# Optimization experiments

Measured on AMD Instinct MI355X. Metric: run time of the kernel, lower is better.

Reference implementation:

```python
import jax, jax.numpy as jnp
import numpy as np

B, S, N = 16, 128, 64            # batch, sentence length, padded KB-word slots per sentence
E, DK, H, L = 128, 128, 128, 32  # char embed, kb embed, per-direction hidden (hidden_size=2H), labels
CHAR_NUM, KB_NUM = 8000, 200000


def setup_inputs():
    key = jax.random.key(0)
    ks = jax.random.split(key, 40)
    u = lambda k, sh: jax.random.uniform(k, sh, jnp.float32, -0.08, 0.08)
    inp = {
        "char_ids": jax.random.randint(ks[0], (B, S), 0, CHAR_NUM),
        "kb_word_ids": jax.random.randint(ks[1], (B, N), 0, KB_NUM),
        "word_begin": jax.random.randint(ks[2], (B, N), 0, S),
        "word_len": jax.random.randint(ks[3], (B, N), 0, 6),
        "label": jax.random.randint(ks[4], (B, S), 0, L),
        "sequence_length": jax.random.randint(ks[5], (B,), S // 2, S + 1),
        "char_emb": u(ks[6], (CHAR_NUM, E)),
        "kb_emb": u(ks[7], (KB_NUM, DK)),
        "dense_W": u(ks[8], (2 * H, L)),
        "dense_b": jnp.zeros((L,), jnp.float32),
        "crf_T": u(ks[9], (L, L)),
    }
    i = 10
    for p in ("f", "r"):
        inp[p + "_Wcx"] = u(ks[i], (E, 4 * H))
        inp[p + "_Wch"] = u(ks[i + 1], (H, 4 * H))
        inp[p + "_bc"] = jnp.zeros((4 * H,), jnp.float32)
        inp[p + "_Wwx"] = u(ks[i + 2], (DK, 3 * H))
        inp[p + "_Wwh"] = u(ks[i + 3], (H, 3 * H))
        inp[p + "_bw"] = jnp.zeros((3 * H,), jnp.float32)
        inp[p + "_Wlx"] = u(ks[i + 4], (E, H))
        inp[p + "_Wlc"] = u(ks[i + 5], (H, H))
        inp[p + "_bl"] = jnp.zeros((H,), jnp.float32)
        i += 6
    return inp


def _lattice_dir(X, Xw, begin, end, pos_valid, word_valid,
                 Wcx, Wch, bc, Wwx, Wwh, bw, Wlx, Wlc, bl):
    # X:[S,E] chars in scan order, Xw:[N,DK] KB words, begin/end:[N] span indices
    # in scan order (end inclusive), pos_valid:[S] bool, word_valid:[N] bool.
    Xg = X @ Wcx + bc    # [S,4H] hoisted char-gate input projection
    Xl = X @ Wlx + bl    # [S,H]  hoisted link-gate input projection
    Wg = Xw @ Wwx + bw   # [N,3H] hoisted word-gate input projection

    def step(carry, t):
        h_hist, c_hist = carry                 # [S+1,H]; slot k = state after step k-1
        h_prev, c_prev = h_hist[t], c_hist[t]
        gi, gf, go, gg = jnp.split(Xg[t] + h_prev @ Wch, 4)
        i = jax.nn.sigmoid(gi); f = jax.nn.sigmoid(gf)
        o = jax.nn.sigmoid(go); g = jnp.tanh(gg)
        # word cells: built from the state just before each word's begin position
        hb, cb = h_hist[begin], c_hist[begin]  # [N,H]
        wi, wf, wg = jnp.split(Wg + hb @ Wwh, 3, axis=1)
        cw = jax.nn.sigmoid(wf) * cb + jax.nn.sigmoid(wi) * jnp.tanh(wg)  # [N,H]
        lg = jax.nn.sigmoid(Xl[t] + cw @ Wlc)  # [N,H] link gates
        wmask = ((end == t) & word_valid).astype(X.dtype)[:, None]
        ew = jnp.exp(lg) * wmask
        ec = jnp.exp(i)
        c_lat = (ec * g + (ew * cw).sum(0)) / (ec + ew.sum(0))  # gate-normalized merge
        c_std = f * c_prev + i * g             # plain LSTM step when no word ends at t
        c_t = jnp.where(wmask.sum() > 0, c_lat, c_std)
        h_t = o * jnp.tanh(c_t)
        v = pos_valid[t]
        h_hist = h_hist.at[t + 1].set(jnp.where(v, h_t, h_prev))
        c_hist = c_hist.at[t + 1].set(jnp.where(v, c_t, c_prev))
        return (h_hist, c_hist), jnp.where(v, h_t, jnp.zeros_like(h_t))

    init = (jnp.zeros((S + 1, H), X.dtype), jnp.zeros((S + 1, H), X.dtype))
    _, hs = jax.lax.scan(step, init, jnp.arange(S))
    return hs  # [S,H]


def _forward(char_ids, kb_word_ids, word_begin, word_len, label, sequence_length,
             char_emb, kb_emb, dense_W, dense_b, crf_T, fparams, rparams):
    X = char_emb[char_ids]            # [B,S,E]
    Xw = kb_emb[kb_word_ids]          # [B,N,DK]
    end = jnp.minimum(word_begin + word_len, S - 1)   # inclusive span end
    word_valid = end < sequence_length[:, None]       # whole span inside sentence
    pos = jnp.arange(S)
    pv_f = pos[None, :] < sequence_length[:, None]
    fwd = jax.vmap(lambda x, xw, b, e, pv, wv:
                   _lattice_dir(x, xw, b, e, pv, wv, *fparams))(
        X, Xw, word_begin, end, pv_f, word_valid)
    # backward direction: flip time axis; span (b,e) maps to (S-1-e, S-1-b)
    pv_r = pos[None, :] >= (S - sequence_length)[:, None]
    bwd = jax.vmap(lambda x, xw, b, e, pv, wv:
                   _lattice_dir(x, xw, b, e, pv, wv, *rparams))(
        X[:, ::-1], Xw, S - 1 - end, S - 1 - word_begin, pv_r, word_valid)[:, ::-1]
    feats = jnp.concatenate([fwd, bwd], axis=-1)      # [B,S,2H]
    logits = feats @ dense_W + dense_b                # [B,S,L]
    # CRF negative log-likelihood
    mask = pv_f.astype(logits.dtype)                  # [B,S]
    emit = jnp.take_along_axis(logits, label[..., None], axis=2)[..., 0]
    trans = crf_T[label[:, :-1], label[:, 1:]]
    gold = (emit * mask).sum(1) + (trans * mask[:, 1:]).sum(1)

    def fstep(alpha, xs):
        logit_t, m_t = xs
        new = jax.scipy.special.logsumexp(alpha[:, :, None] + crf_T[None], axis=1) + logit_t
        return jnp.where(m_t[:, None] > 0, new, alpha), None

    alpha, _ = jax.lax.scan(fstep, logits[:, 0],
                            (logits[:, 1:].transpose(1, 0, 2), mask[:, 1:].T))
    logZ = jax.scipy.special.logsumexp(alpha, axis=1)
    return jnp.mean(logZ - gold)


def reference(char_ids, kb_word_ids, word_begin, word_len, label, sequence_length,
              char_emb, kb_emb, dense_W, dense_b, crf_T,
              f_Wcx, f_Wch, f_bc, f_Wwx, f_Wwh, f_bw, f_Wlx, f_Wlc, f_bl,
              r_Wcx, r_Wch, r_bc, r_Wwx, r_Wwh, r_bw, r_Wlx, r_Wlc, r_bl):
    fparams = (f_Wcx, f_Wch, f_bc, f_Wwx, f_Wwh, f_bw, f_Wlx, f_Wlc, f_bl)
    rparams = (r_Wcx, r_Wch, r_bc, r_Wwx, r_Wwh, r_bw, r_Wlx, r_Wlc, r_bl)
    return _forward(char_ids, kb_word_ids, word_begin, word_len, label, sequence_length,
                    char_emb, kb_emb, dense_W, dense_b, crf_T, fparams, rparams)
```

## Files before the change

kernel.cpp:

```cpp
#include <hip/hip_runtime.h>


typedef _Float16 f16x2 __attribute__((ext_vector_type(2)));

__device__ __forceinline__ float sigm(float x) { return 1.f / (1.f + __expf(-x)); }
__device__ __forceinline__ float tanh_fast(float x) {
    return 1.f - 2.f / (__expf(2.f * x) + 1.f);
}
__device__ __forceinline__ void bar_lgkm() {
    asm volatile("s_waitcnt lgkmcnt(0)\n\ts_barrier" ::: "memory");
}

#if defined(__has_builtin)
#if __has_builtin(__builtin_amdgcn_fdot2)
#define FDOT2(a, b, c) __builtin_amdgcn_fdot2((a), (b), (c), false)
#endif
#endif
#ifndef FDOT2
__device__ __forceinline__ float fdot2_sw(f16x2 a, f16x2 b, float c) {
    return fmaf((float)a.x, (float)b.x, fmaf((float)a.y, (float)b.y, c));
}
#define FDOT2(a, b, c) fdot2_sw((a), (b), (c))
#endif

template <int K, int J, int RPB, int BLK>
__global__ __launch_bounds__(BLK)
void gemm_pair(const float* __restrict__ emb, const int* __restrict__ idx,
               const float* __restrict__ W0, const float* __restrict__ W1,
               const float* __restrict__ b0, const float* __restrict__ b1,
               float* __restrict__ out, int rowsTotal, int Sdim, int revmode)
{
    constexpr int NJ4 = J / 4;
    constexpr int RT  = BLK / NJ4;
    constexpr int RPT = RPB / RT;
    static_assert(BLK % NJ4 == 0 && RPB % RT == 0, "layout");
    const int y = blockIdx.y;
    const float* __restrict__ W    = y ? W1 : W0;
    const float* __restrict__ bias = y ? b1 : b0;
    float* __restrict__ outp = out + (size_t)y * rowsTotal * J;
    const int rev = (revmode && y) ? 1 : 0;

    __shared__ __align__(16) float xs[RPB * K];
    __shared__ const float* srcs[RPB];
    const int tid = threadIdx.x;
    const int r0 = blockIdx.x * RPB;
    if (tid < RPB) {
        const int row = r0 + tid;
        const float* s = nullptr;
        if (row < rowsTotal) {
            if (idx) {
                const int bb = row / Sdim, tt = row - bb * Sdim;
                const int ts = rev ? (Sdim - 1 - tt) : tt;
                s = emb + (size_t)idx[bb * Sdim + ts] * K;
            } else {
                s = emb + (size_t)row * K;
            }
        }
        srcs[tid] = s;
    }
    __syncthreads();
    constexpr int NQ = RPB * K / 4;
    for (int q = tid; q < NQ; q += BLK) {
        const int rr = q / (K / 4), qq = q - rr * (K / 4);
        const float4* s = (const float4*)srcs[rr];
        ((float4*)xs)[q] = s ? s[qq] : make_float4(0.f, 0.f, 0.f, 0.f);
    }
    __syncthreads();

    const int jq = tid % NJ4;
    const int rg = tid / NJ4;
    float4 acc[RPT];
#pragma unroll
    for (int r = 0; r < RPT; ++r) acc[r] = make_float4(0.f, 0.f, 0.f, 0.f);
    const float4* __restrict__ W4 = (const float4*)W;
#pragma unroll 4
    for (int k = 0; k < K; ++k) {
        const float4 wv = W4[(size_t)k * NJ4 + jq];
#pragma unroll
        for (int r = 0; r < RPT; ++r) {
            const float xv = xs[(rg * RPT + r) * K + k];
            acc[r].x = fmaf(xv, wv.x, acc[r].x);
            acc[r].y = fmaf(xv, wv.y, acc[r].y);
            acc[r].z = fmaf(xv, wv.z, acc[r].z);
            acc[r].w = fmaf(xv, wv.w, acc[r].w);
        }
    }
    const float4 bv = ((const float4*)bias)[jq];
#pragma unroll
    for (int r = 0; r < RPT; ++r) {
        const int row = r0 + rg * RPT + r;
        if (row < rowsTotal)
            ((float4*)outp)[(size_t)row * NJ4 + jq] =
                make_float4(acc[r].x + bv.x, acc[r].y + bv.y,
                            acc[r].z + bv.z, acc[r].w + bv.w);
    }
}

#define HH_BYTES (129 * 128 * 2)
#define CH_BYTES (129 * 128 * 4)
#define LAT_DYN_SMEM (HH_BYTES + CH_BYTES)

__global__ __launch_bounds__(512, 2)
void lattice_kernel(const float* __restrict__ Xg,
                    const float* __restrict__ Xl,
                    const float* __restrict__ Wgp,
                    const float* __restrict__ Wch_f, const float* __restrict__ Wch_r,
                    const float* __restrict__ Wwh_f, const float* __restrict__ Wwh_r,
                    const float* __restrict__ Wlc_f, const float* __restrict__ Wlc_r,
                    const int* __restrict__ word_begin, const int* __restrict__ word_len,
                    const int* __restrict__ seqlen,
                    float* __restrict__ feats)
{
    extern __shared__ __align__(16) char dyn_smem[];
    _Float16* hh = (_Float16*)dyn_smem;
    float*    ch = (float*)(dyn_smem + HH_BYTES);

    const int bdid = blockIdx.x;
    const int b = bdid >> 1, dir = bdid & 1;
    const int tid = threadIdx.x;
    const int kc = tid >> 7;
    const int jj = tid & 127;

    const float* Wch = dir ? Wch_r : Wch_f;
    const float* Wwh = dir ? Wwh_r : Wwh_f;
    const float* Wlc = dir ? Wlc_r : Wlc_f;

    f16x2 wch2[64];
    {
        const float* base = Wch + (size_t)(kc * 32) * 512 + jj;
#pragma unroll
        for (int g = 0; g < 4; ++g)
#pragma unroll
            for (int u2 = 0; u2 < 16; ++u2) {
                f16x2 v;
                v.x = (_Float16)base[(size_t)(2 * u2) * 512 + g * 128];
                v.y = (_Float16)base[(size_t)(2 * u2 + 1) * 512 + g * 128];
                wch2[g * 16 + u2] = v;
            }
    }
    f16x2 wwh2[48];
    {
        const float* base = Wwh + (size_t)(kc * 32) * 384 + jj;
#pragma unroll
        for (int g = 0; g < 3; ++g)
#pragma unroll
            for (int u2 = 0; u2 < 16; ++u2) {
                f16x2 v;
                v.x = (_Float16)base[(size_t)(2 * u2) * 384 + g * 128];
                v.y = (_Float16)base[(size_t)(2 * u2 + 1) * 384 + g * 128];
                wwh2[g * 16 + u2] = v;
            }
    }
    f16x2 wlc2[16];
    {
        const float* base = Wlc + (size_t)(kc * 32) * 128 + jj;
#pragma unroll
        for (int u2 = 0; u2 < 16; ++u2) {
            f16x2 v;
            v.x = (_Float16)base[(size_t)(2 * u2) * 128];
            v.y = (_Float16)base[(size_t)(2 * u2 + 1) * 128];
            wlc2[u2] = v;
        }
    }

    __shared__ __align__(16) float part[2048];
    __shared__ __align__(16) float wpart[2 * 1536];
    __shared__ __align__(16) float lpart[2 * 512];
    __shared__ __align__(16) _Float16 cw2s[2 * 128];
    __shared__ int ev_start[129];
    __shared__ int cnts[128];
    __shared__ int fills[128];
    __shared__ short ev_word[64];
    __shared__ short wbeg_s[64];

    const int sl = seqlen[b];

    if (tid < 128) { cnts[tid] = 0; fills[tid] = 0; }
    __syncthreads();
    int myvalid = 0, myed = 0;
    if (tid < 64) {
        const int bg = word_begin[b * 64 + tid];
        const int ln = word_len[b * 64 + tid];
        int ef = bg + ln; if (ef > 127) ef = 127;
        myvalid = (ef < sl);
        const int bd_ = dir ? (127 - ef) : bg;
        const int ed_ = dir ? (127 - bg) : ef;
        wbeg_s[tid] = (short)bd_;
        myed = ed_;
        if (myvalid) atomicAdd(&cnts[ed_], 1);
    }
    __syncthreads();
    if (tid == 0) {
        int run = 0; ev_start[0] = 0;
        for (int t = 0; t < 128; ++t) { run += cnts[t]; ev_start[t + 1] = run; }
    }
    __syncthreads();
    if (tid < 64 && myvalid) {
        const int pos = atomicAdd(&fills[myed], 1);
        ev_word[ev_start[myed] + pos] = (short)tid;
    }
    if (tid < 128) { hh[tid] = (_Float16)0.f; ch[tid] = 0.f; }
    __syncthreads();

    const float* Xg_b = Xg + ((size_t)dir * 2048 + (size_t)b * 128) * 512;
    const float* Xl_b = Xl + ((size_t)dir * 2048 + (size_t)b * 128) * 128;
    const float* Wg_b = Wgp + ((size_t)dir * 1024 + (size_t)b * 64) * 384;

    float h_reg = 0.f, c_reg = 0.f;
    float xg_cur = Xg_b[tid];

    for (int t = 0; t < 128; ++t) {
        const int e0 = ev_start[t];
        const int E  = ev_start[t + 1] - e0;
        const int ec0 = E < 2 ? E : 2;

        int bgs[2] = {0, 0};
        float wgp[2][3];
        float xl = 0.f;
#pragma unroll
        for (int s = 0; s < 2; ++s)
            if (s < ec0) {
                const int w = ev_word[e0 + s];
                bgs[s] = wbeg_s[w];
                if (tid < 128) {
                    const float* wgr = Wg_b + (size_t)w * 384;
                    wgp[s][0] = wgr[tid]; wgp[s][1] = wgr[128 + tid]; wgp[s][2] = wgr[256 + tid];
                }
            }
        if (E > 0 && tid < 128) xl = Xl_b[(size_t)t * 128 + tid];
        const float xg_nxt = (t < 127) ? Xg_b[(size_t)(t + 1) * 512 + tid] : 0.f;

        {
            const f16x2* hrow = (const f16x2*)(hh + (size_t)t * 128) + kc * 16;
            f16x2 hv[16];
#pragma unroll
            for (int u2 = 0; u2 < 16; ++u2) hv[u2] = hrow[u2];
            float p0 = 0.f, p1 = 0.f, p2 = 0.f, p3 = 0.f;
#pragma unroll
            for (int u2 = 0; u2 < 16; ++u2) {
                p0 = FDOT2(wch2[u2],      hv[u2], p0);
                p1 = FDOT2(wch2[16 + u2], hv[u2], p1);
                p2 = FDOT2(wch2[32 + u2], hv[u2], p2);
                p3 = FDOT2(wch2[48 + u2], hv[u2], p3);
            }
            if      (kc == 0) p0 += xg_cur;
            else if (kc == 1) p1 += xg_cur;
            else if (kc == 2) p2 += xg_cur;
            else              p3 += xg_cur;
            part[kc * 512 +       jj] = p0;
            part[kc * 512 + 128 + jj] = p1;
            part[kc * 512 + 256 + jj] = p2;
            part[kc * 512 + 384 + jj] = p3;
        }
#pragma unroll
        for (int s = 0; s < 2; ++s)
            if (s < ec0) {
                const f16x2* hbrow = (const f16x2*)(hh + (size_t)bgs[s] * 128) + kc * 16;
                float q0 = 0.f, q1 = 0.f, q2 = 0.f;
#pragma unroll
                for (int u2 = 0; u2 < 16; ++u2) {
                    const f16x2 hb = hbrow[u2];
                    q0 = FDOT2(wwh2[u2],      hb, q0);
                    q1 = FDOT2(wwh2[16 + u2], hb, q1);
                    q2 = FDOT2(wwh2[32 + u2], hb, q2);
                }
                wpart[s * 1536 + kc * 384 +       jj] = q0;
                wpart[s * 1536 + kc * 384 + 128 + jj] = q1;
                wpart[s * 1536 + kc * 384 + 256 + jj] = q2;
            }
        bar_lgkm();

        float gi = 0.f, gf = 0.f, go = 0.f, gg = 0.f;
        float cwreg[2] = {0.f, 0.f};
        if (tid < 128) {
            const float a0 = part[tid]       + part[512 + tid]  + part[1024 + tid] + part[1536 + tid];
            const float a1 = part[128 + tid] + part[640 + tid]  + part[1152 + tid] + part[1664 + tid];
            const float a2 = part[256 + tid] + part[768 + tid]  + part[1280 + tid] + part[1792 + tid];
            const float a3 = part[384 + tid] + part[896 + tid]  + part[1408 + tid] + part[1920 + tid];
            gi = sigm(a0); gf = sigm(a1); go = sigm(a2); gg = tanh_fast(a3);
#pragma unroll
            for (int s = 0; s < 2; ++s)
                if (s < ec0) {
                    const int sb = s * 1536;
                    const float cb = ch[(size_t)bgs[s] * 128 + tid];
                    const float wi = wgp[s][0] + wpart[sb + tid]       + wpart[sb + 384 + tid] + wpart[sb + 768 + tid]  + wpart[sb + 1152 + tid];
                    const float wf = wgp[s][1] + wpart[sb + 128 + tid] + wpart[sb + 512 + tid] + wpart[sb + 896 + tid]  + wpart[sb + 1280 + tid];
                    const float wv = wgp[s][2] + wpart[sb + 256 + tid] + wpart[sb + 640 + tid] + wpart[sb + 1024 + tid] + wpart[sb + 1408 + tid];
                    const float cwv = sigm(wf) * cb + sigm(wi) * tanh_fast(wv);
                    cwreg[s] = cwv;
                    cw2s[s * 128 + tid] = (_Float16)cwv;
                }
        }

        float accn = 0.f, accd = 0.f;
        if (E > 0) {
            bar_lgkm();
            const int nc = (E + 1) >> 1;
            for (int c = 0; c < nc; ++c) {
                const int base = c * 2;
                const int en = (E - base) < 2 ? (E - base) : 2;
#pragma unroll
                for (int s = 0; s < 2; ++s)
                    if (s < en) {
                        const f16x2* cwrow = (const f16x2*)(cw2s + s * 128) + kc * 16;
                        float r = 0.f;
#pragma unroll
                        for (int u2 = 0; u2 < 16; ++u2) r = FDOT2(wlc2[u2], cwrow[u2], r);
                        lpart[s * 512 + kc * 128 + jj] = r;
                    }
                const int nb = base + 2;
                int nn = E - nb; nn = nn < 0 ? 0 : (nn > 2 ? 2 : nn);
                int bgs2[2] = {0, 0};
                float wgp2[2][3];
#pragma unroll
                for (int s = 0; s < 2; ++s)
                    if (s < nn) {
                        const int w = ev_word[e0 + nb + s];
                        bgs2[s] = wbeg_s[w];
                        if (tid < 128) {
                            const float* wgr = Wg_b + (size_t)w * 384;
                            wgp2[s][0] = wgr[tid]; wgp2[s][1] = wgr[128 + tid]; wgp2[s][2] = wgr[256 + tid];
                        }
                    }
#pragma unroll
                for (int s = 0; s < 2; ++s)
                    if (s < nn) {
                        const f16x2* hbrow = (const f16x2*)(hh + (size_t)bgs2[s] * 128) + kc * 16;
                        float q0 = 0.f, q1 = 0.f, q2 = 0.f;
#pragma unroll
                        for (int u2 = 0; u2 < 16; ++u2) {
                            const f16x2 hb = hbrow[u2];
                            q0 = FDOT2(wwh2[u2],      hb, q0);
                            q1 = FDOT2(wwh2[16 + u2], hb, q1);
                            q2 = FDOT2(wwh2[32 + u2], hb, q2);
                        }
                        wpart[s * 1536 + kc * 384 +       jj] = q0;
                        wpart[s * 1536 + kc * 384 + 128 + jj] = q1;
                        wpart[s * 1536 + kc * 384 + 256 + jj] = q2;
                    }
                bar_lgkm();
                if (tid < 128) {
#pragma unroll
                    for (int s = 0; s < 2; ++s)
                        if (s < en) {
                            const float lg = sigm(xl + lpart[s * 512 + tid] + lpart[s * 512 + 128 + tid]
                                                     + lpart[s * 512 + 256 + tid] + lpart[s * 512 + 384 + tid]);
                            const float ew = __expf(lg);
                            accn = fmaf(ew, cwreg[s], accn);
                            accd += ew;
                        }
#pragma unroll
                    for (int s = 0; s < 2; ++s)
                        if (s < nn) {
                            const int sb = s * 1536;
                            const float cb = ch[(size_t)bgs2[s] * 128 + tid];
                            const float wi = wgp2[s][0] + wpart[sb + tid]       + wpart[sb + 384 + tid] + wpart[sb + 768 + tid]  + wpart[sb + 1152 + tid];
                            const float wf = wgp2[s][1] + wpart[sb + 128 + tid] + wpart[sb + 512 + tid] + wpart[sb + 896 + tid]  + wpart[sb + 1280 + tid];
                            const float wv = wgp2[s][2] + wpart[sb + 256 + tid] + wpart[sb + 640 + tid] + wpart[sb + 1024 + tid] + wpart[sb + 1408 + tid];
                            const float cwv = sigm(wf) * cb + sigm(wi) * tanh_fast(wv);
                            cwreg[s] = cwv;
                            cw2s[s * 128 + tid] = (_Float16)cwv;
                        }
                }
                if (c + 1 < nc) bar_lgkm();
            }
        }

        if (tid < 128) {
            float c_t;
            if (E > 0) {
                const float ec = __expf(gi);
                c_t = (ec * gg + accn) / (ec + accd);
            } else {
                c_t = gf * c_reg + gi * gg;
            }
            const float h_t = go * tanh_fast(c_t);
            const bool v = dir ? (t >= 128 - sl) : (t < sl);
            const float hn = v ? h_t : h_reg;
            const float cn = v ? c_t : c_reg;
            h_reg = hn; c_reg = cn;
            hh[(size_t)(t + 1) * 128 + tid] = (_Float16)hn;
            ch[(size_t)(t + 1) * 128 + tid] = cn;
        }
        xg_cur = xg_nxt;
        bar_lgkm();
    }

    for (int i = tid; i < 128 * 128; i += 512) {
        const int t = i >> 7, j = i & 127;
        const bool v = dir ? (t >= 128 - sl) : (t < sl);
        const float hv = v ? (float)hh[(size_t)(t + 1) * 128 + j] : 0.f;
        const int s = dir ? (127 - t) : t;
        feats[((size_t)b * 128 + s) * 256 + dir * 128 + j] = hv;
    }
}

__global__ void crf_kernel(const float* __restrict__ logits,
                           const int* __restrict__ label,
                           const int* __restrict__ seqlen,
                           const float* __restrict__ T,
                           float* __restrict__ out_part)
{
    const int half = threadIdx.x >> 5;
    const int j    = threadIdx.x & 31;
    const int b    = blockIdx.x * 2 + half;

    float Tc[32];
#pragma unroll
    for (int i = 0; i < 32; ++i) Tc[i] = T[i * 32 + j];

    const float* lg = logits + (size_t)b * 128 * 32;
    const int* lab = label + b * 128;
    const int sl = seqlen[b];

    float g = 0.f;
#pragma unroll
    for (int r = 0; r < 4; ++r) {
        const int t = j + r * 32;
        if (t < sl) {
            g += lg[t * 32 + lab[t]];
            if (t >= 1) g += T[lab[t - 1] * 32 + lab[t]];
        }
    }
#pragma unroll
    for (int m = 16; m; m >>= 1) g += __shfl_xor(g, m, 32);

    __shared__ __align__(16) float alpha_s[2][32];
    float av = lg[j];
    alpha_s[half][j] = av;
    __syncthreads();
    for (int t = 1; t < 128; ++t) {
        float a[32];
        const float4* ap = (const float4*)alpha_s[half];
#pragma unroll
        for (int q = 0; q < 8; ++q) {
            const float4 v = ap[q];
            a[4 * q] = v.x; a[4 * q + 1] = v.y; a[4 * q + 2] = v.z; a[4 * q + 3] = v.w;
        }
        float m = -1e30f;
#pragma unroll
        for (int i = 0; i < 32; ++i) m = fmaxf(m, a[i] + Tc[i]);
        float s = 0.f;
#pragma unroll
        for (int i = 0; i < 32; ++i) s += __expf(a[i] + Tc[i] - m);
        float nv = m + __logf(s) + lg[t * 32 + j];
        if (t >= sl) nv = av;
        av = nv;
        __syncthreads();
        alpha_s[half][j] = av;
        __syncthreads();
    }
    float m2 = av;
#pragma unroll
    for (int m = 16; m; m >>= 1) m2 = fmaxf(m2, __shfl_xor(m2, m, 32));
    float s2 = __expf(av - m2);
#pragma unroll
    for (int m = 16; m; m >>= 1) s2 += __shfl_xor(s2, m, 32);
    if (j == 0) out_part[b] = (m2 + __logf(s2)) - g;
}

__global__ void finalize_kernel(const float* __restrict__ partb, float* __restrict__ out)
{
    if (threadIdx.x == 0 && blockIdx.x == 0) {
        float s = 0.f;
        for (int i = 0; i < 16; i++) s += partb[i];
        out[0] = s * (1.f / 16.f);
    }
}

extern "C" void kernel_launch(void* const* d_in, const int* in_sizes, int n_in,
                              void* d_out, int out_size, void* d_ws, size_t ws_size,
                              hipStream_t stream)
{
    (void)in_sizes; (void)n_in; (void)out_size; (void)ws_size;
    const int*   char_ids    = (const int*)d_in[0];
    const int*   kb_word_ids = (const int*)d_in[1];
    const int*   word_begin  = (const int*)d_in[2];
    const int*   word_len    = (const int*)d_in[3];
    const int*   label       = (const int*)d_in[4];
    const int*   seqlen      = (const int*)d_in[5];
    const float* char_emb    = (const float*)d_in[6];
    const float* kb_emb      = (const float*)d_in[7];
    const float* dense_W     = (const float*)d_in[8];
    const float* dense_b     = (const float*)d_in[9];
    const float* crf_T       = (const float*)d_in[10];
    const float* f_Wcx = (const float*)d_in[11];
    const float* f_Wch = (const float*)d_in[12];
    const float* f_bc  = (const float*)d_in[13];
    const float* f_Wwx = (const float*)d_in[14];
    const float* f_Wwh = (const float*)d_in[15];
    const float* f_bw  = (const float*)d_in[16];
    const float* f_Wlx = (const float*)d_in[17];
    const float* f_Wlc = (const float*)d_in[18];
    const float* f_bl  = (const float*)d_in[19];
    const float* r_Wcx = (const float*)d_in[20];
    const float* r_Wch = (const float*)d_in[21];
    const float* r_bc  = (const float*)d_in[22];
    const float* r_Wwx = (const float*)d_in[23];
    const float* r_Wwh = (const float*)d_in[24];
    const float* r_bw  = (const float*)d_in[25];
    const float* r_Wlx = (const float*)d_in[26];
    const float* r_Wlc = (const float*)d_in[27];
    const float* r_bl  = (const float*)d_in[28];

    float* ws = (float*)d_ws;
    size_t o = 0;
    float* Xg     = ws + o; o += (size_t)2 * 2048 * 512;
    float* Xl     = ws + o; o += (size_t)2 * 2048 * 128;
    float* Wg     = ws + o; o += (size_t)2 * 1024 * 384;
    float* feats  = ws + o; o += (size_t)2048 * 256;
    float* logits = ws + o; o += (size_t)2048 * 32;
    float* partb  = ws + o; o += 16;

    gemm_pair<128, 512, 8, 256><<<dim3(256, 2), 256, 0, stream>>>(
        char_emb, char_ids, f_Wcx, r_Wcx, f_bc, r_bc, Xg, 2048, 128, 1);
    gemm_pair<128, 128, 8, 256><<<dim3(256, 2), 256, 0, stream>>>(
        char_emb, char_ids, f_Wlx, r_Wlx, f_bl, r_bl, Xl, 2048, 128, 1);
    gemm_pair<128, 384, 8, 192><<<dim3(128, 2), 192, 0, stream>>>(
        kb_emb, kb_word_ids, f_Wwx, r_Wwx, f_bw, r_bw, Wg, 1024, 64, 0);

    lattice_kernel<<<32, 512, LAT_DYN_SMEM, stream>>>(
        Xg, Xl, Wg, f_Wch, r_Wch, f_Wwh, r_Wwh, f_Wlc, r_Wlc,
        word_begin, word_len, seqlen, feats);

    gemm_pair<256, 32, 16, 128><<<dim3(128, 1), 128, 0, stream>>>(
        feats, nullptr, dense_W, dense_W, dense_b, dense_b, logits, 2048, 128, 0);
    crf_kernel<<<8, 64, 0, stream>>>(logits, label, seqlen, crf_T, partb);
    finalize_kernel<<<1, 64, 0, stream>>>(partb, (float*)d_out);
}
```

Measured before the change: 540.6 us.

## Move word-cell weights to LDS, ring-buffer h/c history, stream feats per step

The lattice kernel no longer keeps the word-cell recurrent weights (Wwh) in per-thread registers; they are staged once into dynamic LDS as fp16 pairs, which cuts VGPR pressure, and a waves_per_eu attribute is added. The full 129-step h/c history in LDS is replaced by an 8-slot ring window. This is only correct while every word span reaches back fewer than 8 steps, which holds because word_len is below 6. Each step now writes its hidden output straight to feats instead of running a separate copy loop at the end. The projection GEMMs also move to 32-row tiles with fewer blocks. The trade-off is extra LDS reads on the word path in exchange for fewer registers and less end-of-kernel work.

```diff
diff --git a/kernel.cpp b/kernel.cpp
--- a/kernel.cpp
+++ b/kernel.cpp
@@ -96,11 +96,9 @@
     }
 }
 
-#define HH_BYTES (129 * 128 * 2)
-#define CH_BYTES (129 * 128 * 4)
-#define LAT_DYN_SMEM (HH_BYTES + CH_BYTES)
-
-__global__ __launch_bounds__(512, 2)
+#define WWH_LDS_BYTES (64 * 384 * 4)
+
+__global__ __launch_bounds__(512, 2) __attribute__((amdgpu_waves_per_eu(2, 2)))
 void lattice_kernel(const float* __restrict__ Xg,
                     const float* __restrict__ Xl,
                     const float* __restrict__ Wgp,
@@ -112,8 +110,7 @@
                     float* __restrict__ feats)
 {
     extern __shared__ __align__(16) char dyn_smem[];
-    _Float16* hh = (_Float16*)dyn_smem;
-    float*    ch = (float*)(dyn_smem + HH_BYTES);
+    f16x2* wwh_lds = (f16x2*)dyn_smem;
 
     const int bdid = blockIdx.x;
     const int b = bdid >> 1, dir = bdid & 1;
@@ -125,6 +122,14 @@
     const float* Wwh = dir ? Wwh_r : Wwh_f;
     const float* Wlc = dir ? Wlc_r : Wlc_f;
 
+    for (int i = tid; i < 64 * 384; i += 512) {
+        const int k2 = i / 384, col = i - k2 * 384;
+        f16x2 v;
+        v.x = (_Float16)Wwh[(size_t)(2 * k2) * 384 + col];
+        v.y = (_Float16)Wwh[(size_t)(2 * k2 + 1) * 384 + col];
+        wwh_lds[i] = v;
+    }
+
     f16x2 wch2[64];
     {
         const float* base = Wch + (size_t)(kc * 32) * 512 + jj;
@@ -138,19 +143,6 @@
                 wch2[g * 16 + u2] = v;
             }
     }
-    f16x2 wwh2[48];
-    {
-        const float* base = Wwh + (size_t)(kc * 32) * 384 + jj;
-#pragma unroll
-        for (int g = 0; g < 3; ++g)
-#pragma unroll
-            for (int u2 = 0; u2 < 16; ++u2) {
-                f16x2 v;
-                v.x = (_Float16)base[(size_t)(2 * u2) * 384 + g * 128];
-                v.y = (_Float16)base[(size_t)(2 * u2 + 1) * 384 + g * 128];
-                wwh2[g * 16 + u2] = v;
-            }
-    }
     f16x2 wlc2[16];
     {
         const float* base = Wlc + (size_t)(kc * 32) * 128 + jj;
@@ -163,6 +155,8 @@
         }
     }
 
+    __shared__ __align__(16) _Float16 h_win[8][128];
+    __shared__ __align__(16) float    c_win[8][128];
     __shared__ __align__(16) float part[2048];
     __shared__ __align__(16) float wpart[2 * 1536];
     __shared__ __align__(16) float lpart[2 * 512];
@@ -199,12 +193,13 @@
         const int pos = atomicAdd(&fills[myed], 1);
         ev_word[ev_start[myed] + pos] = (short)tid;
     }
-    if (tid < 128) { hh[tid] = (_Float16)0.f; ch[tid] = 0.f; }
+    if (tid < 128) { h_win[0][tid] = (_Float16)0.f; c_win[0][tid] = 0.f; }
     __syncthreads();
 
     const float* Xg_b = Xg + ((size_t)dir * 2048 + (size_t)b * 128) * 512;
     const float* Xl_b = Xl + ((size_t)dir * 2048 + (size_t)b * 128) * 128;
     const float* Wg_b = Wgp + ((size_t)dir * 1024 + (size_t)b * 64) * 384;
+    float* feats_bd = feats + (size_t)b * 128 * 256 + dir * 128;
 
     float h_reg = 0.f, c_reg = 0.f;
     float xg_cur = Xg_b[tid];
@@ -231,7 +226,7 @@
         const float xg_nxt = (t < 127) ? Xg_b[(size_t)(t + 1) * 512 + tid] : 0.f;
 
         {
-            const f16x2* hrow = (const f16x2*)(hh + (size_t)t * 128) + kc * 16;
+            const f16x2* hrow = (const f16x2*)h_win[t & 7] + kc * 16;
             f16x2 hv[16];
 #pragma unroll
             for (int u2 = 0; u2 < 16; ++u2) hv[u2] = hrow[u2];
@@ -255,14 +250,16 @@
 #pragma unroll
         for (int s = 0; s < 2; ++s)
             if (s < ec0) {
-                const f16x2* hbrow = (const f16x2*)(hh + (size_t)bgs[s] * 128) + kc * 16;
+                const f16x2* hbrow = (const f16x2*)h_win[bgs[s] & 7] + kc * 16;
+                const int wb = (kc * 16) * 384 + jj;
                 float q0 = 0.f, q1 = 0.f, q2 = 0.f;
 #pragma unroll
                 for (int u2 = 0; u2 < 16; ++u2) {
                     const f16x2 hb = hbrow[u2];
-                    q0 = FDOT2(wwh2[u2],      hb, q0);
-                    q1 = FDOT2(wwh2[16 + u2], hb, q1);
-                    q2 = FDOT2(wwh2[32 + u2], hb, q2);
+                    const int o = wb + u2 * 384;
+                    q0 = FDOT2(wwh_lds[o],       hb, q0);
+                    q1 = FDOT2(wwh_lds[o + 128], hb, q1);
+                    q2 = FDOT2(wwh_lds[o + 256], hb, q2);
                 }
                 wpart[s * 1536 + kc * 384 +       jj] = q0;
                 wpart[s * 1536 + kc * 384 + 128 + jj] = q1;
@@ -282,7 +279,7 @@
             for (int s = 0; s < 2; ++s)
                 if (s < ec0) {
                     const int sb = s * 1536;
-                    const float cb = ch[(size_t)bgs[s] * 128 + tid];
+                    const float cb = c_win[bgs[s] & 7][tid];
                     const float wi = wgp[s][0] + wpart[sb + tid]       + wpart[sb + 384 + tid] + wpart[sb + 768 + tid]  + wpart[sb + 1152 + tid];
                     const float wf = wgp[s][1] + wpart[sb + 128 + tid] + wpart[sb + 512 + tid] + wpart[sb + 896 + tid]  + wpart[sb + 1280 + tid];
                     const float wv = wgp[s][2] + wpart[sb + 256 + tid] + wpart[sb + 640 + tid] + wpart[sb + 1024 + tid] + wpart[sb + 1408 + tid];
@@ -325,14 +322,16 @@
 #pragma unroll
                 for (int s = 0; s < 2; ++s)
                     if (s < nn) {
-                        const f16x2* hbrow = (const f16x2*)(hh + (size_t)bgs2[s] * 128) + kc * 16;
+                        const f16x2* hbrow = (const f16x2*)h_win[bgs2[s] & 7] + kc * 16;
+                        const int wb = (kc * 16) * 384 + jj;
                         float q0 = 0.f, q1 = 0.f, q2 = 0.f;
 #pragma unroll
                         for (int u2 = 0; u2 < 16; ++u2) {
                             const f16x2 hb = hbrow[u2];
-                            q0 = FDOT2(wwh2[u2],      hb, q0);
-                            q1 = FDOT2(wwh2[16 + u2], hb, q1);
-                            q2 = FDOT2(wwh2[32 + u2], hb, q2);
+                            const int o = wb + u2 * 384;
+                            q0 = FDOT2(wwh_lds[o],       hb, q0);
+                            q1 = FDOT2(wwh_lds[o + 128], hb, q1);
+                            q2 = FDOT2(wwh_lds[o + 256], hb, q2);
                         }
                         wpart[s * 1536 + kc * 384 +       jj] = q0;
                         wpart[s * 1536 + kc * 384 + 128 + jj] = q1;
@@ -353,7 +352,7 @@
                     for (int s = 0; s < 2; ++s)
                         if (s < nn) {
                             const int sb = s * 1536;
-                            const float cb = ch[(size_t)bgs2[s] * 128 + tid];
+                            const float cb = c_win[bgs2[s] & 7][tid];
                             const float wi = wgp2[s][0] + wpart[sb + tid]       + wpart[sb + 384 + tid] + wpart[sb + 768 + tid]  + wpart[sb + 1152 + tid];
                             const float wf = wgp2[s][1] + wpart[sb + 128 + tid] + wpart[sb + 512 + tid] + wpart[sb + 896 + tid]  + wpart[sb + 1280 + tid];
                             const float wv = wgp2[s][2] + wpart[sb + 256 + tid] + wpart[sb + 640 + tid] + wpart[sb + 1024 + tid] + wpart[sb + 1408 + tid];
@@ -379,19 +378,13 @@
             const float hn = v ? h_t : h_reg;
             const float cn = v ? c_t : c_reg;
             h_reg = hn; c_reg = cn;
-            hh[(size_t)(t + 1) * 128 + tid] = (_Float16)hn;
-            ch[(size_t)(t + 1) * 128 + tid] = cn;
+            h_win[(t + 1) & 7][tid] = (_Float16)hn;
+            c_win[(t + 1) & 7][tid] = cn;
+            const int s = dir ? (127 - t) : t;
+            feats_bd[(size_t)s * 256 + tid] = v ? h_t : 0.f;
         }
         xg_cur = xg_nxt;
         bar_lgkm();
-    }
-
-    for (int i = tid; i < 128 * 128; i += 512) {
-        const int t = i >> 7, j = i & 127;
-        const bool v = dir ? (t >= 128 - sl) : (t < sl);
-        const float hv = v ? (float)hh[(size_t)(t + 1) * 128 + j] : 0.f;
-        const int s = dir ? (127 - t) : t;
-        feats[((size_t)b * 128 + s) * 256 + dir * 128 + j] = hv;
     }
 }
 
@@ -512,18 +505,18 @@
     float* logits = ws + o; o += (size_t)2048 * 32;
     float* partb  = ws + o; o += 16;
 
-    gemm_pair<128, 512, 8, 256><<<dim3(256, 2), 256, 0, stream>>>(
+    gemm_pair<128, 512, 32, 256><<<dim3(64, 2), 256, 0, stream>>>(
         char_emb, char_ids, f_Wcx, r_Wcx, f_bc, r_bc, Xg, 2048, 128, 1);
-    gemm_pair<128, 128, 8, 256><<<dim3(256, 2), 256, 0, stream>>>(
+    gemm_pair<128, 128, 32, 256><<<dim3(64, 2), 256, 0, stream>>>(
         char_emb, char_ids, f_Wlx, r_Wlx, f_bl, r_bl, Xl, 2048, 128, 1);
-    gemm_pair<128, 384, 8, 192><<<dim3(128, 2), 192, 0, stream>>>(
+    gemm_pair<128, 384, 32, 192><<<dim3(32, 2), 192, 0, stream>>>(
         kb_emb, kb_word_ids, f_Wwx, r_Wwx, f_bw, r_bw, Wg, 1024, 64, 0);
 
-    lattice_kernel<<<32, 512, LAT_DYN_SMEM, stream>>>(
+    lattice_kernel<<<32, 512, WWH_LDS_BYTES, stream>>>(
         Xg, Xl, Wg, f_Wch, r_Wch, f_Wwh, r_Wwh, f_Wlc, r_Wlc,
         word_begin, word_len, seqlen, feats);
 
-    gemm_pair<256, 32, 16, 128><<<dim3(128, 1), 128, 0, stream>>>(
+    gemm_pair<256, 32, 32, 128><<<dim3(64, 1), 128, 0, stream>>>(
         feats, nullptr, dense_W, dense_W, dense_b, dense_b, logits, 2048, 128, 0);
     crf_kernel<<<8, 64, 0, stream>>>(logits, label, seqlen, crf_T, partb);
     finalize_kernel<<<1, 64, 0, stream>>>(partb, (float*)d_out);
```

Measured after the change: 565.2 us. 4.6% more time.

## Split lattice recurrence K-dim across 1024 threads with cell-state ring buffer

Applied to the files above, without the earlier changes.

Doubles the lattice kernel block from 512 to 1024 threads, so each thread holds half as many recurrent weight registers and reduces a 16-wide slice of the hidden state. Partial sums go through larger shared buffers and an 8-way reduction. The full fp32 cell history is replaced by an 8-row ring buffer, and the Xg prefetch is deepened by one step. The input-projection GEMMs also process more rows per block and unroll the K loop further. The aim is to shorten the serial per-step dot products, at the cost of a longer shared-memory reduction and heavier barriers. The 8-row window is only correct if every word spans fewer than 8 steps, which holds here since word_len is at most 5.

```diff
diff --git a/kernel.cpp b/kernel.cpp
--- a/kernel.cpp
+++ b/kernel.cpp
@@ -73,7 +73,7 @@
 #pragma unroll
     for (int r = 0; r < RPT; ++r) acc[r] = make_float4(0.f, 0.f, 0.f, 0.f);
     const float4* __restrict__ W4 = (const float4*)W;
-#pragma unroll 4
+#pragma unroll 8
     for (int k = 0; k < K; ++k) {
         const float4 wv = W4[(size_t)k * NJ4 + jq];
 #pragma unroll
@@ -96,11 +96,7 @@
     }
 }
 
-#define HH_BYTES (129 * 128 * 2)
-#define CH_BYTES (129 * 128 * 4)
-#define LAT_DYN_SMEM (HH_BYTES + CH_BYTES)
-
-__global__ __launch_bounds__(512, 2)
+__global__ __launch_bounds__(1024, 4)
 void lattice_kernel(const float* __restrict__ Xg,
                     const float* __restrict__ Xl,
                     const float* __restrict__ Wgp,
@@ -111,51 +107,48 @@
                     const int* __restrict__ seqlen,
                     float* __restrict__ feats)
 {
-    extern __shared__ __align__(16) char dyn_smem[];
-    _Float16* hh = (_Float16*)dyn_smem;
-    float*    ch = (float*)(dyn_smem + HH_BYTES);
-
     const int bdid = blockIdx.x;
     const int b = bdid >> 1, dir = bdid & 1;
     const int tid = threadIdx.x;
     const int kc = tid >> 7;
     const int jj = tid & 127;
+    const int koff = kc * 16;
 
     const float* Wch = dir ? Wch_r : Wch_f;
     const float* Wwh = dir ? Wwh_r : Wwh_f;
     const float* Wlc = dir ? Wlc_r : Wlc_f;
 
-    f16x2 wch2[64];
+    f16x2 wch2[32];
     {
-        const float* base = Wch + (size_t)(kc * 32) * 512 + jj;
+        const float* base = Wch + (size_t)koff * 512 + jj;
 #pragma unroll
         for (int g = 0; g < 4; ++g)
 #pragma unroll
-            for (int u2 = 0; u2 < 16; ++u2) {
+            for (int u2 = 0; u2 < 8; ++u2) {
                 f16x2 v;
                 v.x = (_Float16)base[(size_t)(2 * u2) * 512 + g * 128];
                 v.y = (_Float16)base[(size_t)(2 * u2 + 1) * 512 + g * 128];
-                wch2[g * 16 + u2] = v;
-            }
-    }
-    f16x2 wwh2[48];
+                wch2[g * 8 + u2] = v;
+            }
+    }
+    f16x2 wwh2[24];
     {
-        const float* base = Wwh + (size_t)(kc * 32) * 384 + jj;
+        const float* base = Wwh + (size_t)koff * 384 + jj;
 #pragma unroll
         for (int g = 0; g < 3; ++g)
 #pragma unroll
-            for (int u2 = 0; u2 < 16; ++u2) {
+            for (int u2 = 0; u2 < 8; ++u2) {
                 f16x2 v;
                 v.x = (_Float16)base[(size_t)(2 * u2) * 384 + g * 128];
                 v.y = (_Float16)base[(size_t)(2 * u2 + 1) * 384 + g * 128];
-                wwh2[g * 16 + u2] = v;
-            }
-    }
-    f16x2 wlc2[16];
+                wwh2[g * 8 + u2] = v;
+            }
+    }
+    f16x2 wlc2[8];
     {
-        const float* base = Wlc + (size_t)(kc * 32) * 128 + jj;
-#pragma unroll
-        for (int u2 = 0; u2 < 16; ++u2) {
+        const float* base = Wlc + (size_t)koff * 128 + jj;
+#pragma unroll
+        for (int u2 = 0; u2 < 8; ++u2) {
             f16x2 v;
             v.x = (_Float16)base[(size_t)(2 * u2) * 128];
             v.y = (_Float16)base[(size_t)(2 * u2 + 1) * 128];
@@ -163,9 +156,11 @@
         }
     }
 
-    __shared__ __align__(16) float part[2048];
-    __shared__ __align__(16) float wpart[2 * 1536];
-    __shared__ __align__(16) float lpart[2 * 512];
+    __shared__ __align__(16) _Float16 hh[129 * 128];
+    __shared__ __align__(16) float    c_win[8 * 128];
+    __shared__ __align__(16) float part[8 * 512];
+    __shared__ __align__(16) float wpart[2 * 3072];
+    __shared__ __align__(16) float lpart[2 * 1024];
     __shared__ __align__(16) _Float16 cw2s[2 * 128];
     __shared__ int ev_start[129];
     __shared__ int cnts[128];
@@ -199,7 +194,7 @@
         const int pos = atomicAdd(&fills[myed], 1);
         ev_word[ev_start[myed] + pos] = (short)tid;
     }
-    if (tid < 128) { hh[tid] = (_Float16)0.f; ch[tid] = 0.f; }
+    if (tid < 128) { hh[tid] = (_Float16)0.f; c_win[tid] = 0.f; }
     __syncthreads();
 
     const float* Xg_b = Xg + ((size_t)dir * 2048 + (size_t)b * 128) * 512;
@@ -207,13 +202,15 @@
     const float* Wg_b = Wgp + ((size_t)dir * 1024 + (size_t)b * 64) * 384;
 
     float h_reg = 0.f, c_reg = 0.f;
-    float xg_cur = Xg_b[tid];
+    float xg_cur = (tid < 512) ? Xg_b[tid] : 0.f;
+    float xg_n1  = (tid < 512) ? Xg_b[512 + tid] : 0.f;
 
     for (int t = 0; t < 128; ++t) {
         const int e0 = ev_start[t];
         const int E  = ev_start[t + 1] - e0;
         const int ec0 = E < 2 ? E : 2;
 
+        const float xg_n2 = (t + 2 < 128 && tid < 512) ? Xg_b[(size_t)(t + 2) * 512 + tid] : 0.f;
         int bgs[2] = {0, 0};
         float wgp[2][3];
         float xl = 0.f;
@@ -228,25 +225,24 @@
                 }
             }
         if (E > 0 && tid < 128) xl = Xl_b[(size_t)t * 128 + tid];
-        const float xg_nxt = (t < 127) ? Xg_b[(size_t)(t + 1) * 512 + tid] : 0.f;
 
         {
-            const f16x2* hrow = (const f16x2*)(hh + (size_t)t * 128) + kc * 16;
-            f16x2 hv[16];
-#pragma unroll
-            for (int u2 = 0; u2 < 16; ++u2) hv[u2] = hrow[u2];
+            const f16x2* hrow = (const f16x2*)(hh + (size_t)t * 128) + kc * 8;
+            f16x2 hv[8];
+#pragma unroll
+            for (int u2 = 0; u2 < 8; ++u2) hv[u2] = hrow[u2];
             float p0 = 0.f, p1 = 0.f, p2 = 0.f, p3 = 0.f;
 #pragma unroll
-            for (int u2 = 0; u2 < 16; ++u2) {
+            for (int u2 = 0; u2 < 8; ++u2) {
                 p0 = FDOT2(wch2[u2],      hv[u2], p0);
-                p1 = FDOT2(wch2[16 + u2], hv[u2], p1);
-                p2 = FDOT2(wch2[32 + u2], hv[u2], p2);
-                p3 = FDOT2(wch2[48 + u2], hv[u2], p3);
+                p1 = FDOT2(wch2[8 + u2],  hv[u2], p1);
+                p2 = FDOT2(wch2[16 + u2], hv[u2], p2);
+                p3 = FDOT2(wch2[24 + u2], hv[u2], p3);
             }
             if      (kc == 0) p0 += xg_cur;
             else if (kc == 1) p1 += xg_cur;
             else if (kc == 2) p2 += xg_cur;
-            else              p3 += xg_cur;
+            else if (kc == 3) p3 += xg_cur;
             part[kc * 512 +       jj] = p0;
             part[kc * 512 + 128 + jj] = p1;
             part[kc * 512 + 256 + jj] = p2;
@@ -255,37 +251,45 @@
 #pragma unroll
         for (int s = 0; s < 2; ++s)
             if (s < ec0) {
-                const f16x2* hbrow = (const f16x2*)(hh + (size_t)bgs[s] * 128) + kc * 16;
+                const f16x2* hbrow = (const f16x2*)(hh + (size_t)bgs[s] * 128) + kc * 8;
                 float q0 = 0.f, q1 = 0.f, q2 = 0.f;
 #pragma unroll
-                for (int u2 = 0; u2 < 16; ++u2) {
+                for (int u2 = 0; u2 < 8; ++u2) {
                     const f16x2 hb = hbrow[u2];
                     q0 = FDOT2(wwh2[u2],      hb, q0);
-                    q1 = FDOT2(wwh2[16 + u2], hb, q1);
-                    q2 = FDOT2(wwh2[32 + u2], hb, q2);
+                    q1 = FDOT2(wwh2[8 + u2],  hb, q1);
+                    q2 = FDOT2(wwh2[16 + u2], hb, q2);
                 }
-                wpart[s * 1536 + kc * 384 +       jj] = q0;
-                wpart[s * 1536 + kc * 384 + 128 + jj] = q1;
-                wpart[s * 1536 + kc * 384 + 256 + jj] = q2;
+                wpart[s * 3072 + kc * 384 +       jj] = q0;
+                wpart[s * 3072 + kc * 384 + 128 + jj] = q1;
+                wpart[s * 3072 + kc * 384 + 256 + jj] = q2;
             }
         bar_lgkm();
 
         float gi = 0.f, gf = 0.f, go = 0.f, gg = 0.f;
         float cwreg[2] = {0.f, 0.f};
         if (tid < 128) {
-            const float a0 = part[tid]       + part[512 + tid]  + part[1024 + tid] + part[1536 + tid];
-            const float a1 = part[128 + tid] + part[640 + tid]  + part[1152 + tid] + part[1664 + tid];
-            const float a2 = part[256 + tid] + part[768 + tid]  + part[1280 + tid] + part[1792 + tid];
-            const float a3 = part[384 + tid] + part[896 + tid]  + part[1408 + tid] + part[1920 + tid];
+            float a0 = 0.f, a1 = 0.f, a2 = 0.f, a3 = 0.f;
+#pragma unroll
+            for (int k8 = 0; k8 < 8; ++k8) {
+                a0 += part[k8 * 512 +       tid];
+                a1 += part[k8 * 512 + 128 + tid];
+                a2 += part[k8 * 512 + 256 + tid];
+                a3 += part[k8 * 512 + 384 + tid];
+            }
             gi = sigm(a0); gf = sigm(a1); go = sigm(a2); gg = tanh_fast(a3);
 #pragma unroll
             for (int s = 0; s < 2; ++s)
                 if (s < ec0) {
-                    const int sb = s * 1536;
-                    const float cb = ch[(size_t)bgs[s] * 128 + tid];
-                    const float wi = wgp[s][0] + wpart[sb + tid]       + wpart[sb + 384 + tid] + wpart[sb + 768 + tid]  + wpart[sb + 1152 + tid];
-                    const float wf = wgp[s][1] + wpart[sb + 128 + tid] + wpart[sb + 512 + tid] + wpart[sb + 896 + tid]  + wpart[sb + 1280 + tid];
-                    const float wv = wgp[s][2] + wpart[sb + 256 + tid] + wpart[sb + 640 + tid] + wpart[sb + 1024 + tid] + wpart[sb + 1408 + tid];
+                    const int sb = s * 3072;
+                    float wi = wgp[s][0], wf = wgp[s][1], wv = wgp[s][2];
+#pragma unroll
+                    for (int k8 = 0; k8 < 8; ++k8) {
+                        wi += wpart[sb + k8 * 384 +       tid];
+                        wf += wpart[sb + k8 * 384 + 128 + tid];
+                        wv += wpart[sb + k8 * 384 + 256 + tid];
+                    }
+                    const float cb = c_win[(bgs[s] & 7) * 128 + tid];
                     const float cwv = sigm(wf) * cb + sigm(wi) * tanh_fast(wv);
                     cwreg[s] = cwv;
                     cw2s[s * 128 + tid] = (_Float16)cwv;
@@ -302,11 +306,11 @@
 #pragma unroll
                 for (int s = 0; s < 2; ++s)
                     if (s < en) {
-                        const f16x2* cwrow = (const f16x2*)(cw2s + s * 128) + kc * 16;
+                        const f16x2* cwrow = (const f16x2*)(cw2s + s * 128) + kc * 8;
                         float r = 0.f;
 #pragma unroll
-                        for (int u2 = 0; u2 < 16; ++u2) r = FDOT2(wlc2[u2], cwrow[u2], r);
-                        lpart[s * 512 + kc * 128 + jj] = r;
+                        for (int u2 = 0; u2 < 8; ++u2) r = FDOT2(wlc2[u2], cwrow[u2], r);
+                        lpart[s * 1024 + kc * 128 + jj] = r;
                     }
                 const int nb = base + 2;
                 int nn = E - nb; nn = nn < 0 ? 0 : (nn > 2 ? 2 : nn);
@@ -325,26 +329,28 @@
 #pragma unroll
                 for (int s = 0; s < 2; ++s)
                     if (s < nn) {
-                        const f16x2* hbrow = (const f16x2*)(hh + (size_t)bgs2[s] * 128) + kc * 16;
+                        const f16x2* hbrow = (const f16x2*)(hh + (size_t)bgs2[s] * 128) + kc * 8;
                         float q0 = 0.f, q1 = 0.f, q2 = 0.f;
 #pragma unroll
-                        for (int u2 = 0; u2 < 16; ++u2) {
+                        for (int u2 = 0; u2 < 8; ++u2) {
                             const f16x2 hb = hbrow[u2];
                             q0 = FDOT2(wwh2[u2],      hb, q0);
-                            q1 = FDOT2(wwh2[16 + u2], hb, q1);
-                            q2 = FDOT2(wwh2[32 + u2], hb, q2);
+                            q1 = FDOT2(wwh2[8 + u2],  hb, q1);
+                            q2 = FDOT2(wwh2[16 + u2], hb, q2);
                         }
-                        wpart[s * 1536 + kc * 384 +       jj] = q0;
-                        wpart[s * 1536 + kc * 384 + 128 + jj] = q1;
-                        wpart[s * 1536 + kc * 384 + 256 + jj] = q2;
+                        wpart[s * 3072 + kc * 384 +       jj] = q0;
+                        wpart[s * 3072 + kc * 384 + 128 + jj] = q1;
+                        wpart[s * 3072 + kc * 384 + 256 + jj] = q2;
                     }
                 bar_lgkm();
                 if (tid < 128) {
 #pragma unroll
                     for (int s = 0; s < 2; ++s)
                         if (s < en) {
-                            const float lg = sigm(xl + lpart[s * 512 + tid] + lpart[s * 512 + 128 + tid]
-                                                     + lpart[s * 512 + 256 + tid] + lpart[s * 512 + 384 + tid]);
+                            float lsum = xl;
+#pragma unroll
+                            for (int k8 = 0; k8 < 8; ++k8) lsum += lpart[s * 1024 + k8 * 128 + tid];
+                            const float lg = sigm(lsum);
                             const float ew = __expf(lg);
                             accn = fmaf(ew, cwreg[s], accn);
                             accd += ew;
@@ -352,11 +358,15 @@
 #pragma unroll
                     for (int s = 0; s < 2; ++s)
                         if (s < nn) {
-                            const int sb = s * 1536;
-                            const float cb = ch[(size_t)bgs2[s] * 128 + tid];
-                            const float wi = wgp2[s][0] + wpart[sb + tid]       + wpart[sb + 384 + tid] + wpart[sb + 768 + tid]  + wpart[sb + 1152 + tid];
-                            const float wf = wgp2[s][1] + wpart[sb + 128 + tid] + wpart[sb + 512 + tid] + wpart[sb + 896 + tid]  + wpart[sb + 1280 + tid];
-                            const float wv = wgp2[s][2] + wpart[sb + 256 + tid] + wpart[sb + 640 + tid] + wpart[sb + 1024 + tid] + wpart[sb + 1408 + tid];
+                            const int sb = s * 3072;
+                            float wi = wgp2[s][0], wf = wgp2[s][1], wv = wgp2[s][2];
+#pragma unroll
+                            for (int k8 = 0; k8 < 8; ++k8) {
+                                wi += wpart[sb + k8 * 384 +       tid];
+                                wf += wpart[sb + k8 * 384 + 128 + tid];
+                                wv += wpart[sb + k8 * 384 + 256 + tid];
+                            }
+                            const float cb = c_win[(bgs2[s] & 7) * 128 + tid];
                             const float cwv = sigm(wf) * cb + sigm(wi) * tanh_fast(wv);
                             cwreg[s] = cwv;
                             cw2s[s * 128 + tid] = (_Float16)cwv;
@@ -380,13 +390,14 @@
             const float cn = v ? c_t : c_reg;
             h_reg = hn; c_reg = cn;
             hh[(size_t)(t + 1) * 128 + tid] = (_Float16)hn;
-            ch[(size_t)(t + 1) * 128 + tid] = cn;
-        }
-        xg_cur = xg_nxt;
+            c_win[((t + 1) & 7) * 128 + tid] = cn;
+        }
+        xg_cur = xg_n1;
+        xg_n1  = xg_n2;
         bar_lgkm();
     }
 
-    for (int i = tid; i < 128 * 128; i += 512) {
+    for (int i = tid; i < 128 * 128; i += 1024) {
         const int t = i >> 7, j = i & 127;
         const bool v = dir ? (t >= 128 - sl) : (t < sl);
         const float hv = v ? (float)hh[(size_t)(t + 1) * 128 + j] : 0.f;
@@ -512,14 +523,14 @@
     float* logits = ws + o; o += (size_t)2048 * 32;
     float* partb  = ws + o; o += 16;
 
-    gemm_pair<128, 512, 8, 256><<<dim3(256, 2), 256, 0, stream>>>(
+    gemm_pair<128, 512, 16, 256><<<dim3(128, 2), 256, 0, stream>>>(
         char_emb, char_ids, f_Wcx, r_Wcx, f_bc, r_bc, Xg, 2048, 128, 1);
-    gemm_pair<128, 128, 8, 256><<<dim3(256, 2), 256, 0, stream>>>(
+    gemm_pair<128, 128, 16, 256><<<dim3(128, 2), 256, 0, stream>>>(
         char_emb, char_ids, f_Wlx, r_Wlx, f_bl, r_bl, Xl, 2048, 128, 1);
-    gemm_pair<128, 384, 8, 192><<<dim3(128, 2), 192, 0, stream>>>(
+    gemm_pair<128, 384, 16, 192><<<dim3(64, 2), 192, 0, stream>>>(
         kb_emb, kb_word_ids, f_Wwx, r_Wwx, f_bw, r_bw, Wg, 1024, 64, 0);
 
-    lattice_kernel<<<32, 512, LAT_DYN_SMEM, stream>>>(
+    lattice_kernel<<<32, 1024, 0, stream>>>(
         Xg, Xl, Wg, f_Wch, r_Wch, f_Wwh, r_Wwh, f_Wlc, r_Wlc,
         word_begin, word_len, seqlen, feats);
 
```

New measurement: 660.9 us. 22.3% more time.
